# Kernel tuning notes

Hardware: AMD Instinct MI355X
Metric: run time of the kernel (lower is better)

The kernel has to match this reference:

```python
import jax, jax.numpy as jnp
import numpy as np

B, NL, H, C = 256, 128, 64, 64
N_GENES, G = 30000, 5000
BN_EPS = 1e-5


def setup_inputs() -> dict:
    key = jax.random.key(0)
    ks = jax.random.split(key, 10)
    stdv_lin = 1.0 / np.sqrt(NL)
    stdv_w = 1.0 / np.sqrt(H)  # matches uniform_(-stdv, stdv) on weight table
    return {
        "latent": jax.random.normal(ks[0], (B, NL), dtype=jnp.float32),
        "genes_oi": jax.random.randint(ks[1], (G,), 0, N_GENES, dtype=jnp.int32),
        "W1": jax.random.uniform(ks[2], (NL, H), jnp.float32, -stdv_lin, stdv_lin),
        "b1": jax.random.uniform(ks[3], (H,), jnp.float32, -stdv_lin, stdv_lin),
        "bn_gamma": jnp.ones((H,), jnp.float32),
        "bn_beta": jnp.zeros((H,), jnp.float32),
        "bn_mean": jax.random.normal(ks[4], (H,), jnp.float32) * 0.1,
        "bn_var": jax.random.uniform(ks[5], (H,), jnp.float32, 0.5, 1.5),
        "weight_table": jax.random.uniform(ks[6], (N_GENES, H, C), jnp.float32, -stdv_w, stdv_w),
        "bias_table": jnp.zeros((N_GENES, C), jnp.float32),
    }


def reference(latent, genes_oi, W1, b1, bn_gamma, bn_beta, bn_mean, bn_var,
              weight_table, bias_table):
    # MLP stack: Linear -> ReLU -> BatchNorm1d (eval: running stats) -> Dropout (eval: identity)
    h = jax.nn.relu(latent @ W1 + b1)                       # [B, H]
    h = (h - bn_mean) * jax.lax.rsqrt(bn_var + BN_EPS) * bn_gamma + bn_beta
    # Per-gene gathered weight/bias, then broadcast batched matmul + bias
    w = weight_table[genes_oi]                              # [G, H, C]
    b = bias_table[genes_oi]                                # [G, C]
    out = jnp.einsum("bh,ghc->bgc", h, w) + b               # [B, G, C]
    return out
```

## Files before the change

### kernel.cpp

```cpp
#include <hip/hip_runtime.h>
#include <hip/hip_bf16.h>

#define BB 256
#define NLAT 128
#define HH 64
#define CC 64
#define GG 5000
#define NG 4
#define NBLK (GG / NG)
#define GSTRIDE (GG * CC)
#define BN_EPS 1e-5f

typedef __bf16 bf16x8 __attribute__((ext_vector_type(8)));
typedef float f32x4 __attribute__((ext_vector_type(4)));

__global__ void hprep_kernel(const float* __restrict__ latent,
                             const float* __restrict__ W1,
                             const float* __restrict__ b1,
                             const float* __restrict__ gamma,
                             const float* __restrict__ beta,
                             const float* __restrict__ mean,
                             const float* __restrict__ var,
                             unsigned short* __restrict__ hout) {
    const int b = blockIdx.x;
    const int c = threadIdx.x;
    float acc = b1[c];
    const float* lrow = latent + b * NLAT;
#pragma unroll 8
    for (int k = 0; k < NLAT; ++k)
        acc = fmaf(lrow[k], W1[k * HH + c], acc);
    acc = fmaxf(acc, 0.f);
    float s = gamma[c] * rsqrtf(var[c] + BN_EPS);
    acc = (acc - mean[c]) * s + beta[c];
    __bf16 hv = (__bf16)acc;
    hout[b * HH + c] = *reinterpret_cast<unsigned short*>(&hv);
}

__device__ __forceinline__ void barrier_lds_only() {
    asm volatile("s_waitcnt lgkmcnt(0)" ::: "memory");
    __builtin_amdgcn_s_barrier();
    asm volatile("" ::: "memory");
}

__global__ __launch_bounds__(512, 4) void decoder_kernel(
    const unsigned short* __restrict__ hbuf,
    const int* __restrict__ genes,
    const float* __restrict__ wt,
    const float* __restrict__ bt,
    float* __restrict__ out)
{
    __shared__ __align__(16) unsigned short ldsW[2][4096];
    __shared__ __align__(16) float ldsO[BB * CC];

    const int tid = threadIdx.x;
    const int l   = tid & 63;
    const int w   = tid >> 6;
    const int l16 = l & 15;
    const int lg  = l >> 4;

    const int xcd = blockIdx.x & 7;
    const int k   = blockIdx.x >> 3;
    const int v   = (xcd < 2 ? xcd * 157 : 314 + (xcd - 2) * 156) + k;
    const int g0  = v * NG;

    bf16x8 afrag[2][2];
#pragma unroll
    for (int m = 0; m < 2; ++m)
#pragma unroll
        for (int ks = 0; ks < 2; ++ks) {
            int row = w * 32 + m * 16 + l16;
            afrag[m][ks] = *reinterpret_cast<const bf16x8*>(
                hbuf + row * HH + ks * 32 + lg * 8);
        }

    const int sc  = l;
    const int shb = w;
    const int swz16 = sc * 8 + (shb ^ (sc & 7));

    float pkv[8];

    {
        const float* Wg = wt + (size_t)genes[g0] * (HH * CC);
#pragma unroll
        for (int j = 0; j < 8; ++j)
            pkv[j] = Wg[(shb * 8 + j) * CC + sc];
        bf16x8 pk;
#pragma unroll
        for (int j = 0; j < 8; ++j) pk[j] = (__bf16)pkv[j];
        *reinterpret_cast<bf16x8*>(
            reinterpret_cast<char*>(ldsW[0]) + swz16 * 16) = pk;
    }
    barrier_lds_only();

    int p = 0;
#pragma unroll
    for (int i = 0; i < NG; ++i) {
        const int g = g0 + i;

        if (i + 1 < NG) {
            const float* Wn = wt + (size_t)genes[g + 1] * (HH * CC);
#pragma unroll
            for (int j = 0; j < 8; ++j)
                pkv[j] = Wn[(shb * 8 + j) * CC + sc];
        }

        const float* bg = bt + (size_t)genes[g] * CC;
        const char* buf = reinterpret_cast<const char*>(ldsW[p]);
        f32x4 E[4][2];
#pragma unroll
        for (int n = 0; n < 4; ++n) {
            const int c = n * 16 + l16;
            bf16x8 bfr0 = *reinterpret_cast<const bf16x8*>(
                buf + (c * 8 + ((0 + lg) ^ (c & 7))) * 16);
            bf16x8 bfr1 = *reinterpret_cast<const bf16x8*>(
                buf + (c * 8 + ((4 + lg) ^ (c & 7))) * 16);
            f32x4 binit = *reinterpret_cast<const f32x4*>(bg + n * 16 + lg * 4);
#pragma unroll
            for (int m = 0; m < 2; ++m) {
                f32x4 e = binit;
                e = __builtin_amdgcn_mfma_f32_16x16x32_bf16(bfr0, afrag[m][0], e, 0, 0, 0);
                e = __builtin_amdgcn_mfma_f32_16x16x32_bf16(bfr1, afrag[m][1], e, 0, 0, 0);
                E[n][m] = e;
            }
        }

#pragma unroll
        for (int n = 0; n < 4; ++n)
#pragma unroll
            for (int m = 0; m < 2; ++m) {
                int b = w * 32 + m * 16 + l16;
                int qp = (n * 4 + lg) ^ l16;
                *reinterpret_cast<f32x4*>(ldsO + b * CC + qp * 4) = E[n][m];
            }
        barrier_lds_only();

        {
            float* og = out + (size_t)g * CC;
#pragma unroll
            for (int it = 0; it < 8; ++it) {
                int b  = it * 32 + w * 4 + lg;
                int qp = l16 ^ (b & 15);
                f32x4 vv = *reinterpret_cast<const f32x4*>(ldsO + b * CC + qp * 4);
                __builtin_nontemporal_store(
                    vv, reinterpret_cast<f32x4*>(og + (size_t)b * GSTRIDE + l16 * 4));
            }
        }

        if (i + 1 < NG) {
            bf16x8 pk;
#pragma unroll
            for (int j = 0; j < 8; ++j) pk[j] = (__bf16)pkv[j];
            *reinterpret_cast<bf16x8*>(
                reinterpret_cast<char*>(ldsW[p ^ 1]) + swz16 * 16) = pk;
            p ^= 1;
        }
        barrier_lds_only();
    }
}

extern "C" void kernel_launch(void* const* d_in, const int* in_sizes, int n_in,
                              void* d_out, int out_size, void* d_ws, size_t ws_size,
                              hipStream_t stream) {
    const float* latent = (const float*)d_in[0];
    const int*   genes  = (const int*)d_in[1];
    const float* W1     = (const float*)d_in[2];
    const float* b1     = (const float*)d_in[3];
    const float* gamma  = (const float*)d_in[4];
    const float* beta   = (const float*)d_in[5];
    const float* mean   = (const float*)d_in[6];
    const float* var    = (const float*)d_in[7];
    const float* wt     = (const float*)d_in[8];
    const float* bt     = (const float*)d_in[9];
    float* out = (float*)d_out;
    unsigned short* hbuf = (unsigned short*)d_ws;

    hprep_kernel<<<dim3(BB), dim3(HH), 0, stream>>>(latent, W1, b1, gamma, beta,
                                                    mean, var, hbuf);
    decoder_kernel<<<dim3(NBLK), dim3(512), 0, stream>>>(hbuf, genes, wt, bt, out);
}
```

Baseline: 77.10 us.

## Prefetch all gene weights and biases up front with nontemporal loads, stage bias in LDS

```diff
diff --git a/kernel.cpp b/kernel.cpp
--- a/kernel.cpp
+++ b/kernel.cpp
@@ -50,6 +50,7 @@
     float* __restrict__ out)
 {
     __shared__ __align__(16) unsigned short ldsW[2][4096];
+    __shared__ __align__(16) float ldsB[2][CC];
     __shared__ __align__(16) float ldsO[BB * CC];
 
     const int tid = threadIdx.x;
@@ -77,19 +78,27 @@
     const int shb = w;
     const int swz16 = sc * 8 + (shb ^ (sc & 7));
 
-    float pkv[8];
-
-    {
-        const float* Wg = wt + (size_t)genes[g0] * (HH * CC);
+    float pkv[NG][8];
+    float bbs[NG];
+#pragma unroll
+    for (int ge = 0; ge < NG; ++ge) {
+        const float* Wg = wt + (size_t)genes[g0 + ge] * (HH * CC);
 #pragma unroll
         for (int j = 0; j < 8; ++j)
-            pkv[j] = Wg[(shb * 8 + j) * CC + sc];
-        bf16x8 pk;
+            pkv[ge][j] =
+                __builtin_nontemporal_load(&Wg[(shb * 8 + j) * CC + sc]);
+        bbs[ge] = __builtin_nontemporal_load(&bt[(size_t)genes[g0 + ge] * CC + l]);
+    }
+    bf16x8 pkb[NG];
 #pragma unroll
-        for (int j = 0; j < 8; ++j) pk[j] = (__bf16)pkv[j];
-        *reinterpret_cast<bf16x8*>(
-            reinterpret_cast<char*>(ldsW[0]) + swz16 * 16) = pk;
-    }
+    for (int ge = 0; ge < NG; ++ge)
+#pragma unroll
+        for (int j = 0; j < 8; ++j)
+            pkb[ge][j] = (__bf16)pkv[ge][j];
+
+    *reinterpret_cast<bf16x8*>(
+        reinterpret_cast<char*>(ldsW[0]) + swz16 * 16) = pkb[0];
+    if (w == 0) ldsB[0][l] = bbs[0];
     barrier_lds_only();
 
     int p = 0;
@@ -97,14 +106,6 @@
     for (int i = 0; i < NG; ++i) {
         const int g = g0 + i;
 
-        if (i + 1 < NG) {
-            const float* Wn = wt + (size_t)genes[g + 1] * (HH * CC);
-#pragma unroll
-            for (int j = 0; j < 8; ++j)
-                pkv[j] = Wn[(shb * 8 + j) * CC + sc];
-        }
-
-        const float* bg = bt + (size_t)genes[g] * CC;
         const char* buf = reinterpret_cast<const char*>(ldsW[p]);
         f32x4 E[4][2];
 #pragma unroll
@@ -114,7 +115,7 @@
                 buf + (c * 8 + ((0 + lg) ^ (c & 7))) * 16);
             bf16x8 bfr1 = *reinterpret_cast<const bf16x8*>(
                 buf + (c * 8 + ((4 + lg) ^ (c & 7))) * 16);
-            f32x4 binit = *reinterpret_cast<const f32x4*>(bg + n * 16 + lg * 4);
+            f32x4 binit = *reinterpret_cast<const f32x4*>(&ldsB[p][n * 16 + lg * 4]);
 #pragma unroll
             for (int m = 0; m < 2; ++m) {
                 f32x4 e = binit;
@@ -147,11 +148,9 @@
         }
 
         if (i + 1 < NG) {
-            bf16x8 pk;
-#pragma unroll
-            for (int j = 0; j < 8; ++j) pk[j] = (__bf16)pkv[j];
             *reinterpret_cast<bf16x8*>(
-                reinterpret_cast<char*>(ldsW[p ^ 1]) + swz16 * 16) = pk;
+                reinterpret_cast<char*>(ldsW[p ^ 1]) + swz16 * 16) = pkb[i + 1];
+            if (w == 0) ldsB[p ^ 1][l] = bbs[i + 1];
             p ^= 1;
         }
         barrier_lds_only();
```

Measured after the change: 95.08 us. 23.3% more time.
